# Performance work log

Hardware: AMD Instinct MI355X
Metric: run time of the kernel (lower is better)

## Reference

```python
import jax, jax.numpy as jnp
import numpy as np

B, F, N = 8, 64, 100000
R = 32
EPS = 1e-6


def setup_inputs() -> dict:
    key = jax.random.key(0)
    k1, k2 = jax.random.split(key)
    features = jax.random.normal(k1, (B, F, N), dtype=jnp.float32)
    coords = jax.random.normal(k2, (B, 3, N), dtype=jnp.float32)
    return {"features": features, "coords": coords}


def _voxelize(coords):
    # coords: [B, 3, N]; original detaches coords -> stop_gradient
    c = jax.lax.stop_gradient(coords)
    # center per-point-cloud (mean over points)
    nc = c - jnp.mean(c, axis=2, keepdims=True)
    # scale by max point radius so cloud fits in [0,1]
    radius = jnp.max(jnp.linalg.norm(nc, axis=1, keepdims=True), axis=2, keepdims=True)  # [B,1,1]
    nc = nc / (radius * 2.0 + EPS) + 0.5
    norm_coords = jnp.clip(nc * R, 0.0, R - 1)  # [B,3,N]
    vox_coords = jnp.round(norm_coords).astype(jnp.int32)
    return vox_coords, norm_coords


def _avg_voxelize(features, vox_coords):
    # features: [B,F,N], vox_coords: [B,3,N] int32 in [0,R)
    b, f, n = features.shape
    # flat voxel index x*R*R + y*R + z, offset per batch element
    idx = (vox_coords[:, 0] * R + vox_coords[:, 1]) * R + vox_coords[:, 2]  # [B,N]
    flat_idx = (idx + jnp.arange(b, dtype=jnp.int32)[:, None] * (R ** 3)).reshape(-1)  # [B*N]
    feat = features.transpose(0, 2, 1).reshape(b * n, f)  # [B*N, F]
    num_seg = b * R ** 3
    sums = jax.ops.segment_sum(feat, flat_idx, num_segments=num_seg)          # [B*R^3, F]
    cnts = jax.ops.segment_sum(jnp.ones((b * n,), feat.dtype), flat_idx, num_segments=num_seg)
    avg = sums / jnp.maximum(cnts, 1.0)[:, None]  # empty voxels stay 0
    return avg.reshape(b, R, R, R, f).transpose(0, 4, 1, 2, 3)  # [B,F,R,R,R]


def reference(features, coords):
    vox_coords, norm_coords = _voxelize(coords)
    grid = _avg_voxelize(features, vox_coords)
    return grid, norm_coords
```

## Files before the change

kernel.cpp:

```cpp
#include <hip/hip_runtime.h>
#include <hip/hip_bf16.h>

#define BB 8
#define FF 64
#define NPTS 100000
#define RES 32
#define R3 (RES*RES*RES)
#define EPSV 1e-6f
#define SEGS (BB*R3)
#define NPTS_TOT (BB*NPTS)
#define NWIN (NPTS_TOT/64)

static constexpr size_t GRID_ELEMS = (size_t)BB * FF * R3;

__device__ __forceinline__ float bf16f(ushort u) {
    return __uint_as_float((unsigned)u << 16);
}

#define NB_STAT 64
__global__ void k_sum_coords(const float* __restrict__ coords, float* __restrict__ sums) {
    int b = blockIdx.x / NB_STAT;
    int chunk = blockIdx.x % NB_STAT;
    const float* cb = coords + (size_t)b * 3 * NPTS;
    float sx = 0.f, sy = 0.f, sz = 0.f;
    for (int i = chunk * blockDim.x + threadIdx.x; i < NPTS; i += NB_STAT * blockDim.x) {
        sx += cb[i];
        sy += cb[NPTS + i];
        sz += cb[2 * NPTS + i];
    }
    for (int off = 32; off; off >>= 1) {
        sx += __shfl_down(sx, off);
        sy += __shfl_down(sy, off);
        sz += __shfl_down(sz, off);
    }
    __shared__ float lsx[4], lsy[4], lsz[4];
    int lane = threadIdx.x & 63, wid = threadIdx.x >> 6;
    if (lane == 0) { lsx[wid] = sx; lsy[wid] = sy; lsz[wid] = sz; }
    __syncthreads();
    if (threadIdx.x == 0) {
        float tx = 0.f, ty = 0.f, tz = 0.f;
        for (int w = 0; w < 4; ++w) { tx += lsx[w]; ty += lsy[w]; tz += lsz[w]; }
        atomicAdd(&sums[b * 3 + 0], tx);
        atomicAdd(&sums[b * 3 + 1], ty);
        atomicAdd(&sums[b * 3 + 2], tz);
    }
}

__global__ void k_radius(const float* __restrict__ coords, const float* __restrict__ sums,
                         int* __restrict__ rad_bits) {
    int b = blockIdx.x / NB_STAT;
    int chunk = blockIdx.x % NB_STAT;
    const float* cb = coords + (size_t)b * 3 * NPTS;
    float mx = sums[b * 3 + 0] / (float)NPTS;
    float my = sums[b * 3 + 1] / (float)NPTS;
    float mz = sums[b * 3 + 2] / (float)NPTS;
    float mval = 0.f;
    for (int i = chunk * blockDim.x + threadIdx.x; i < NPTS; i += NB_STAT * blockDim.x) {
        float x = cb[i] - mx;
        float y = cb[NPTS + i] - my;
        float z = cb[2 * NPTS + i] - mz;
        float nrm = sqrtf(x * x + y * y + z * z);
        mval = fmaxf(mval, nrm);
    }
    for (int off = 32; off; off >>= 1) mval = fmaxf(mval, __shfl_down(mval, off));
    __shared__ float lm[4];
    int lane = threadIdx.x & 63, wid = threadIdx.x >> 6;
    if (lane == 0) lm[wid] = mval;
    __syncthreads();
    if (threadIdx.x == 0) {
        float t = fmaxf(fmaxf(lm[0], lm[1]), fmaxf(lm[2], lm[3]));
        atomicMax(&rad_bits[b], __float_as_int(t));
    }
}

__global__ void k_voxelize(const float* __restrict__ coords, const float* __restrict__ sums,
                           const int* __restrict__ rad_bits, float* __restrict__ norm_out,
                           int* __restrict__ voxidx, int* __restrict__ counts) {
    int tid = blockIdx.x * blockDim.x + threadIdx.x;
    if (tid >= NPTS_TOT) return;
    int b = tid / NPTS, n = tid % NPTS;
    const float* cb = coords + (size_t)b * 3 * NPTS;
    float mx = sums[b * 3 + 0] / (float)NPTS;
    float my = sums[b * 3 + 1] / (float)NPTS;
    float mz = sums[b * 3 + 2] / (float)NPTS;
    float r = __int_as_float(rad_bits[b]);
    float d = 2.0f * r + EPSV;
    float x = (cb[n] - mx) / d + 0.5f;
    float y = (cb[NPTS + n] - my) / d + 0.5f;
    float z = (cb[2 * NPTS + n] - mz) / d + 0.5f;
    float nx = fminf(fmaxf(x * (float)RES, 0.0f), (float)(RES - 1));
    float ny = fminf(fmaxf(y * (float)RES, 0.0f), (float)(RES - 1));
    float nz = fminf(fmaxf(z * (float)RES, 0.0f), (float)(RES - 1));
    float* nb_ = norm_out + (size_t)b * 3 * NPTS;
    nb_[n] = nx;
    nb_[NPTS + n] = ny;
    nb_[2 * NPTS + n] = nz;
    int vx = (int)rintf(nx), vy = (int)rintf(ny), vz = (int)rintf(nz);
    int idx = (vx * RES + vy) * RES + vz;
    voxidx[tid] = idx;
    atomicAdd(&counts[b * R3 + idx], 1);
}

__global__ void k_scan1(const int* __restrict__ counts, int* __restrict__ offsets,
                        int* __restrict__ blocksums) {
    int tid = threadIdx.x, bid = blockIdx.x;
    int base = bid * 1024 + tid * 4;
    int c0 = counts[base], c1 = counts[base + 1], c2 = counts[base + 2], c3 = counts[base + 3];
    int tot = c0 + c1 + c2 + c3;
    int lane = tid & 63, wid = tid >> 6;
    int v = tot;
    for (int off = 1; off < 64; off <<= 1) {
        int u = __shfl_up(v, off);
        if (lane >= off) v += u;
    }
    __shared__ int wtot[4];
    if (lane == 63) wtot[wid] = v;
    __syncthreads();
    int wof = 0;
    for (int w = 0; w < wid; ++w) wof += wtot[w];
    int ex = wof + v - tot;
    offsets[base] = ex;
    offsets[base + 1] = ex + c0;
    offsets[base + 2] = ex + c0 + c1;
    offsets[base + 3] = ex + c0 + c1 + c2;
    if (tid == 0) blocksums[bid] = wtot[0] + wtot[1] + wtot[2] + wtot[3];
}

__global__ void k_scan2(const int* __restrict__ blocksums, int* __restrict__ blockoff) {
    int tid = threadIdx.x;
    int c = blocksums[tid];
    int lane = tid & 63, wid = tid >> 6;
    int v = c;
    for (int off = 1; off < 64; off <<= 1) {
        int u = __shfl_up(v, off);
        if (lane >= off) v += u;
    }
    __shared__ int wtot[4];
    if (lane == 63) wtot[wid] = v;
    __syncthreads();
    int wof = 0;
    for (int w = 0; w < wid; ++w) wof += wtot[w];
    blockoff[tid] = wof + v - c;
}

__global__ void k_fillvox(const int* __restrict__ offsets, const int* __restrict__ blockoff,
                          const int* __restrict__ counts, int* __restrict__ rowvox) {
    int bv = blockIdx.x * 256 + threadIdx.x;
    if (bv >= SEGS) return;
    int off = offsets[bv] + blockoff[bv >> 10];
    int cnt = counts[bv];
    for (int i = 0; i < cnt; ++i) rowvox[off + i] = bv;
}

__global__ void k_transpose_scatter(const float* __restrict__ features,
                                    const int* __restrict__ voxidx,
                                    const int* __restrict__ offsets,
                                    const int* __restrict__ blockoff,
                                    int* __restrict__ cursors,
                                    __hip_bfloat16* __restrict__ featS) {
    __shared__ float tileF[64][65];
    __shared__ int dst[64];
    int b = blockIdx.y;
    int n0 = blockIdx.x * 64;
    int tid = threadIdx.x, lane = tid & 63, wid = tid >> 6;

    for (int f = wid; f < 64; f += 4) {
        int n = n0 + lane;
        tileF[f][lane] = (n < NPTS) ? features[((size_t)b * FF + f) * NPTS + n] : 0.f;
    }
    if (tid < 64) {
        int n = n0 + tid;
        if (n < NPTS) {
            int v = voxidx[(size_t)b * NPTS + n];
            int bv = b * R3 + v;
            int r = atomicAdd(&cursors[bv], 1);
            dst[tid] = offsets[bv] + blockoff[bv >> 10] + r;
        } else {
            dst[tid] = -1;
        }
    }
    __syncthreads();
    for (int p = wid; p < 64; p += 4) {
        int d = dst[p];
        if (d >= 0) featS[(size_t)d * 64 + lane] = __float2bfloat16(tileF[lane][p]);
    }
}

__global__ void k_gather_lin(const ushort* __restrict__ featS,
                             const int* __restrict__ rowvox,
                             const int* __restrict__ counts,
                             float* __restrict__ avgbuf) {
    __shared__ ushort tile[4][4096];
    int wid = threadIdx.x >> 6, lane = threadIdx.x & 63;
    int w = blockIdx.x * 4 + wid;
    int r0 = w * 64;

    const uint4* gsrc = (const uint4*)(featS + (size_t)r0 * 64);
    uint4* ldst = (uint4*)tile[wid];
    uint4 t[8];
#pragma unroll
    for (int j = 0; j < 8; ++j) t[j] = gsrc[j * 64 + lane];
#pragma unroll
    for (int j = 0; j < 8; ++j) ldst[j * 64 + lane] = t[j];

    int myrow = r0 + lane;
    int myv = rowvox[myrow];
    int prevv = __shfl_up(myv, 1);
    int pv0 = (r0 > 0) ? rowvox[r0 - 1] : -1;
    if (lane == 0) prevv = pv0;
    unsigned long long flags = __ballot(myv != prevv);

    while (flags) {
        int s = (int)__ffsll(flags) - 1;
        flags &= flags - 1;
        int bv = __shfl(myv, s);
        int cnt = flags ? ((int)__ffsll(flags) - 1 - s) : counts[bv];
        int inwin = min(cnt, 64 - s);
        float acc = 0.f;
        for (int i = 0; i < inwin; ++i) acc += bf16f(tile[wid][(s + i) * 64 + lane]);
        if (cnt > inwin) {
            const ushort* p = featS + (size_t)(r0 + 64) * 64 + lane;
            int rem = cnt - inwin;
            float b0 = 0.f, b1 = 0.f, b2 = 0.f, b3 = 0.f;
            int i = 0;
            for (; i + 4 <= rem; i += 4) {
                b0 += bf16f(p[(size_t)(i + 0) * 64]);
                b1 += bf16f(p[(size_t)(i + 1) * 64]);
                b2 += bf16f(p[(size_t)(i + 2) * 64]);
                b3 += bf16f(p[(size_t)(i + 3) * 64]);
            }
            for (; i < rem; ++i) b0 += bf16f(p[(size_t)i * 64]);
            acc += (b0 + b1) + (b2 + b3);
        }
        avgbuf[(size_t)bv * 64 + lane] = acc / (float)cnt;
    }
}

__global__ void k_avg2grid(const float* __restrict__ avgbuf, const int* __restrict__ counts,
                           float* __restrict__ grid) {
    __shared__ float tile[64][65];
    int bv0 = blockIdx.x * 64;
    int lane = threadIdx.x & 63, wid = threadIdx.x >> 6;
    for (int p = wid; p < 64; p += 4) {
        int cnt = counts[bv0 + p];
        tile[p][lane] = (cnt > 0) ? avgbuf[(size_t)(bv0 + p) * 64 + lane] : 0.f;
    }
    __syncthreads();
    int b = bv0 >> 15;
    int v0 = bv0 & (R3 - 1);
    for (int f = wid; f < 64; f += 4) {
        grid[((size_t)b * FF + f) * R3 + v0 + lane] = tile[lane][f];
    }
}

__global__ void k_scatter(const float* __restrict__ features, const int* __restrict__ voxidx,
                          float* __restrict__ grid) {
    size_t tid = (size_t)blockIdx.x * blockDim.x + threadIdx.x;
    if (tid >= (size_t)BB * FF * NPTS) return;
    int n = (int)(tid % NPTS);
    int bf = (int)(tid / NPTS);
    int b = bf >> 6;
    int idx = voxidx[(size_t)b * NPTS + n];
    atomicAdd(&grid[(size_t)bf * R3 + idx], features[tid]);
}

__global__ void k_normalize(float* __restrict__ grid, const int* __restrict__ counts) {
    size_t tid = (size_t)blockIdx.x * blockDim.x + threadIdx.x;
    if (tid >= GRID_ELEMS) return;
    int v = (int)(tid % R3);
    int bf = (int)(tid / R3);
    int b = bf >> 6;
    float c = (float)counts[b * R3 + v];
    grid[tid] = grid[tid] / fmaxf(c, 1.0f);
}

extern "C" void kernel_launch(void* const* d_in, const int* in_sizes, int n_in,
                              void* d_out, int out_size, void* d_ws, size_t ws_size,
                              hipStream_t stream) {
    const float* features = (const float*)d_in[0];
    const float* coords = (const float*)d_in[1];
    float* out = (float*)d_out;
    float* grid = out;
    float* norm_out = out + GRID_ELEMS;

    char* ws = (char*)d_ws;
    size_t off_sums   = 0;
    size_t off_rad    = 128;
    size_t off_counts = 256;
    size_t off_offs   = off_counts + (size_t)SEGS * 4;
    size_t off_curs   = off_offs + (size_t)SEGS * 4;
    size_t off_bsums  = off_curs + (size_t)SEGS * 4;
    size_t off_boff   = off_bsums + 256 * 4;
    size_t off_vox    = off_boff + 256 * 4;
    size_t off_rowv   = off_vox + (size_t)NPTS_TOT * 4;
    size_t off_featS  = (off_rowv + (size_t)NPTS_TOT * 4 + 255) & ~(size_t)255;
    size_t off_avg    = (off_featS + (size_t)NPTS_TOT * FF * 2 + 255) & ~(size_t)255;
    size_t needed     = off_avg + (size_t)SEGS * FF * 4;

    float* sums    = (float*)(ws + off_sums);
    int* rad_bits  = (int*)(ws + off_rad);
    int* counts    = (int*)(ws + off_counts);
    int* offsets   = (int*)(ws + off_offs);
    int* cursors   = (int*)(ws + off_curs);
    int* blocksums = (int*)(ws + off_bsums);
    int* blockoff  = (int*)(ws + off_boff);
    int* voxidx    = (int*)(ws + off_vox);
    int* rowvox    = (int*)(ws + off_rowv);
    __hip_bfloat16* featS = (__hip_bfloat16*)(ws + off_featS);
    float* avgbuf  = (float*)(ws + off_avg);

    bool fast = (ws_size >= needed);

    if (fast) {
        hipMemsetAsync(ws, 0, off_bsums, stream);
    } else {
        hipMemsetAsync(ws, 0, off_offs, stream);
        hipMemsetAsync(grid, 0, GRID_ELEMS * sizeof(float), stream);
    }

    k_sum_coords<<<BB * NB_STAT, 256, 0, stream>>>(coords, sums);
    k_radius<<<BB * NB_STAT, 256, 0, stream>>>(coords, sums, rad_bits);

    int pts_blocks = (NPTS_TOT + 255) / 256;
    k_voxelize<<<pts_blocks, 256, 0, stream>>>(coords, sums, rad_bits, norm_out, voxidx, counts);

    if (fast) {
        k_scan1<<<256, 256, 0, stream>>>(counts, offsets, blocksums);
        k_scan2<<<1, 256, 0, stream>>>(blocksums, blockoff);
        k_fillvox<<<(SEGS + 255) / 256, 256, 0, stream>>>(offsets, blockoff, counts, rowvox);
        dim3 tgrid((NPTS + 63) / 64, BB);
        k_transpose_scatter<<<tgrid, 256, 0, stream>>>(features, voxidx, offsets, blockoff,
                                                       cursors, featS);
        k_gather_lin<<<NWIN / 4, 256, 0, stream>>>((const ushort*)featS, rowvox, counts, avgbuf);
        k_avg2grid<<<SEGS / 64, 256, 0, stream>>>(avgbuf, counts, grid);
    } else {
        size_t scatter_threads = (size_t)BB * FF * NPTS;
        int scatter_blocks = (int)((scatter_threads + 255) / 256);
        k_scatter<<<scatter_blocks, 256, 0, stream>>>(features, voxidx, grid);
        int norm_blocks = (int)((GRID_ELEMS + 255) / 256);
        k_normalize<<<norm_blocks, 256, 0, stream>>>(grid, counts);
    }
}
```

Baseline: 289.1 us.

## Replace scattered feature writes with permutation-based gather and bf16 averages

Splits the transpose-scatter into a rank kernel that builds a sorted permutation of point indices and a plain transpose that writes features point-major in bf16 with packed coalesced stores. The gather kernel then reads rows through the permutation instead of reading a pre-sorted buffer. The intent is to replace random 128-byte row scatters with coalesced writes and move the randomness onto reads. The per-voxel averages are also stored as bf16 to halve that intermediate's traffic. This adds one extra kernel launch, an indirect load per row, and extra rounding of the averages.

```diff
diff --git a/kernel.cpp b/kernel.cpp
--- a/kernel.cpp
+++ b/kernel.cpp
@@ -15,6 +15,10 @@
 
 __device__ __forceinline__ float bf16f(ushort u) {
     return __uint_as_float((unsigned)u << 16);
+}
+__device__ __forceinline__ ushort f2bf(float f) {
+    __hip_bfloat16 h = __float2bfloat16(f);
+    return *reinterpret_cast<ushort*>(&h);
 }
 
 #define NB_STAT 64
@@ -152,14 +156,19 @@
     for (int i = 0; i < cnt; ++i) rowvox[off + i] = bv;
 }
 
-__global__ void k_transpose_scatter(const float* __restrict__ features,
-                                    const int* __restrict__ voxidx,
-                                    const int* __restrict__ offsets,
-                                    const int* __restrict__ blockoff,
-                                    int* __restrict__ cursors,
-                                    __hip_bfloat16* __restrict__ featS) {
+__global__ void k_rank(const int* __restrict__ voxidx, const int* __restrict__ offsets,
+                       const int* __restrict__ blockoff, int* __restrict__ cursors,
+                       int* __restrict__ perm) {
+    int g = blockIdx.x * 256 + threadIdx.x;
+    if (g >= NPTS_TOT) return;
+    int b = g / NPTS;
+    int bv = b * R3 + voxidx[g];
+    int r = atomicAdd(&cursors[bv], 1);
+    perm[offsets[bv] + blockoff[bv >> 10] + r] = g;
+}
+
+__global__ void k_transpose(const float* __restrict__ features, ushort* __restrict__ featT) {
     __shared__ float tileF[64][65];
-    __shared__ int dst[64];
     int b = blockIdx.y;
     int n0 = blockIdx.x * 64;
     int tid = threadIdx.x, lane = tid & 63, wid = tid >> 6;
@@ -168,46 +177,46 @@
         int n = n0 + lane;
         tileF[f][lane] = (n < NPTS) ? features[((size_t)b * FF + f) * NPTS + n] : 0.f;
     }
-    if (tid < 64) {
-        int n = n0 + tid;
-        if (n < NPTS) {
-            int v = voxidx[(size_t)b * NPTS + n];
-            int bv = b * R3 + v;
-            int r = atomicAdd(&cursors[bv], 1);
-            dst[tid] = offsets[bv] + blockoff[bv >> 10] + r;
-        } else {
-            dst[tid] = -1;
+    __syncthreads();
+    size_t g0 = (size_t)b * NPTS + n0;
+    int half = lane >> 5;
+    int f0 = (lane & 31) * 2;
+#pragma unroll
+    for (int k = 0; k < 8; ++k) {
+        int p = wid * 16 + k * 2 + half;
+        if (n0 + p < NPTS) {
+            unsigned val = (unsigned)f2bf(tileF[f0][p]) | ((unsigned)f2bf(tileF[f0 + 1][p]) << 16);
+            ((unsigned*)(featT + ((g0 + p) << 6)))[lane & 31] = val;
         }
     }
-    __syncthreads();
-    for (int p = wid; p < 64; p += 4) {
-        int d = dst[p];
-        if (d >= 0) featS[(size_t)d * 64 + lane] = __float2bfloat16(tileF[lane][p]);
-    }
-}
-
-__global__ void k_gather_lin(const ushort* __restrict__ featS,
+}
+
+__global__ void k_gather_lin(const ushort* __restrict__ featT,
+                             const int* __restrict__ perm,
                              const int* __restrict__ rowvox,
                              const int* __restrict__ counts,
-                             float* __restrict__ avgbuf) {
+                             ushort* __restrict__ avgS) {
     __shared__ ushort tile[4][4096];
     int wid = threadIdx.x >> 6, lane = threadIdx.x & 63;
     int w = blockIdx.x * 4 + wid;
     int r0 = w * 64;
 
-    const uint4* gsrc = (const uint4*)(featS + (size_t)r0 * 64);
-    uint4* ldst = (uint4*)tile[wid];
+    int pr = perm[r0 + lane];
+    int myv = rowvox[r0 + lane];
+
     uint4 t[8];
 #pragma unroll
-    for (int j = 0; j < 8; ++j) t[j] = gsrc[j * 64 + lane];
+    for (int j = 0; j < 8; ++j) {
+        int row = j * 8 + (lane >> 3);
+        int pi = __shfl(pr, row);
+        t[j] = ((const uint4*)(featT + ((size_t)pi << 6)))[lane & 7];
+    }
+    uint4* ldst = (uint4*)tile[wid];
 #pragma unroll
     for (int j = 0; j < 8; ++j) ldst[j * 64 + lane] = t[j];
 
-    int myrow = r0 + lane;
-    int myv = rowvox[myrow];
     int prevv = __shfl_up(myv, 1);
-    int pv0 = (r0 > 0) ? rowvox[r0 - 1] : -1;
-    if (lane == 0) prevv = pv0;
+    if (lane == 0) prevv = (r0 > 0) ? rowvox[r0 - 1] : -1;
     unsigned long long flags = __ballot(myv != prevv);
 
     while (flags) {
@@ -219,31 +228,24 @@
         float acc = 0.f;
         for (int i = 0; i < inwin; ++i) acc += bf16f(tile[wid][(s + i) * 64 + lane]);
         if (cnt > inwin) {
-            const ushort* p = featS + (size_t)(r0 + 64) * 64 + lane;
             int rem = cnt - inwin;
-            float b0 = 0.f, b1 = 0.f, b2 = 0.f, b3 = 0.f;
-            int i = 0;
-            for (; i + 4 <= rem; i += 4) {
-                b0 += bf16f(p[(size_t)(i + 0) * 64]);
-                b1 += bf16f(p[(size_t)(i + 1) * 64]);
-                b2 += bf16f(p[(size_t)(i + 2) * 64]);
-                b3 += bf16f(p[(size_t)(i + 3) * 64]);
+            for (int i = 0; i < rem; ++i) {
+                int pi2 = perm[r0 + 64 + i];
+                acc += bf16f(featT[((size_t)pi2 << 6) + lane]);
             }
-            for (; i < rem; ++i) b0 += bf16f(p[(size_t)i * 64]);
-            acc += (b0 + b1) + (b2 + b3);
         }
-        avgbuf[(size_t)bv * 64 + lane] = acc / (float)cnt;
-    }
-}
-
-__global__ void k_avg2grid(const float* __restrict__ avgbuf, const int* __restrict__ counts,
+        avgS[(size_t)bv * 64 + lane] = f2bf(acc / (float)cnt);
+    }
+}
+
+__global__ void k_avg2grid(const ushort* __restrict__ avgS, const int* __restrict__ counts,
                            float* __restrict__ grid) {
     __shared__ float tile[64][65];
     int bv0 = blockIdx.x * 64;
     int lane = threadIdx.x & 63, wid = threadIdx.x >> 6;
     for (int p = wid; p < 64; p += 4) {
         int cnt = counts[bv0 + p];
-        tile[p][lane] = (cnt > 0) ? avgbuf[(size_t)(bv0 + p) * 64 + lane] : 0.f;
+        tile[p][lane] = (cnt > 0) ? bf16f(avgS[(size_t)(bv0 + p) * 64 + lane]) : 0.f;
     }
     __syncthreads();
     int b = bv0 >> 15;
@@ -293,9 +295,10 @@
     size_t off_boff   = off_bsums + 256 * 4;
     size_t off_vox    = off_boff + 256 * 4;
     size_t off_rowv   = off_vox + (size_t)NPTS_TOT * 4;
-    size_t off_featS  = (off_rowv + (size_t)NPTS_TOT * 4 + 255) & ~(size_t)255;
-    size_t off_avg    = (off_featS + (size_t)NPTS_TOT * FF * 2 + 255) & ~(size_t)255;
-    size_t needed     = off_avg + (size_t)SEGS * FF * 4;
+    size_t off_perm   = off_rowv + (size_t)NPTS_TOT * 4;
+    size_t off_featT  = (off_perm + (size_t)NPTS_TOT * 4 + 255) & ~(size_t)255;
+    size_t off_avg    = (off_featT + (size_t)NPTS_TOT * FF * 2 + 255) & ~(size_t)255;
+    size_t needed     = off_avg + (size_t)SEGS * FF * 2;
 
     float* sums    = (float*)(ws + off_sums);
     int* rad_bits  = (int*)(ws + off_rad);
@@ -306,8 +309,9 @@
     int* blockoff  = (int*)(ws + off_boff);
     int* voxidx    = (int*)(ws + off_vox);
     int* rowvox    = (int*)(ws + off_rowv);
-    __hip_bfloat16* featS = (__hip_bfloat16*)(ws + off_featS);
-    float* avgbuf  = (float*)(ws + off_avg);
+    int* perm      = (int*)(ws + off_perm);
+    ushort* featT  = (ushort*)(ws + off_featT);
+    ushort* avgS   = (ushort*)(ws + off_avg);
 
     bool fast = (ws_size >= needed);
 
@@ -328,11 +332,11 @@
         k_scan1<<<256, 256, 0, stream>>>(counts, offsets, blocksums);
         k_scan2<<<1, 256, 0, stream>>>(blocksums, blockoff);
         k_fillvox<<<(SEGS + 255) / 256, 256, 0, stream>>>(offsets, blockoff, counts, rowvox);
+        k_rank<<<pts_blocks, 256, 0, stream>>>(voxidx, offsets, blockoff, cursors, perm);
         dim3 tgrid((NPTS + 63) / 64, BB);
-        k_transpose_scatter<<<tgrid, 256, 0, stream>>>(features, voxidx, offsets, blockoff,
-                                                       cursors, featS);
-        k_gather_lin<<<NWIN / 4, 256, 0, stream>>>((const ushort*)featS, rowvox, counts, avgbuf);
-        k_avg2grid<<<SEGS / 64, 256, 0, stream>>>(avgbuf, counts, grid);
+        k_transpose<<<tgrid, 256, 0, stream>>>(features, featT);
+        k_gather_lin<<<NWIN / 4, 256, 0, stream>>>(featT, perm, rowvox, counts, avgS);
+        k_avg2grid<<<SEGS / 64, 256, 0, stream>>>(avgS, counts, grid);
     } else {
         size_t scatter_threads = (size_t)BB * FF * NPTS;
         int scatter_blocks = (int)((scatter_threads + 255) / 256);
```

Result: slower. 393.4 us (+36.1%).
